# Performance work log

Measured on AMD Instinct MI355X. Metric: run time of the kernel, lower is better.

The kernel has to match this reference:

```python
import jax, jax.numpy as jnp
import numpy as np

B, T, L, D = 2, 16, 256, 1152
NH, HD = 16, 72
MLP_H = int(int(D * 4.0) * 2 / 3)  # 3072, per SwiGLUFFN


def _rms(x, w, eps=1e-6):
    return x * jax.lax.rsqrt(jnp.mean(jnp.square(x), axis=-1, keepdims=True) + eps) * w


def _attn(x, qkv_w, qkv_b, qn, kn, proj_w, proj_b, nh):
    Bn, N, C = x.shape
    hd = C // nh
    qkv = (x @ qkv_w + qkv_b).reshape(Bn, N, 3, nh, hd)
    qkv = jnp.transpose(qkv, (2, 0, 3, 1, 4))  # [3, Bn, nh, N, hd]
    q, k, v = qkv[0], qkv[1], qkv[2]
    q = _rms(q, qn)
    k = _rms(k, kn)
    scores = jnp.einsum('bhnd,bhmd->bhnm', q, k) / jnp.sqrt(jnp.float32(hd))
    a = jax.nn.softmax(scores, axis=-1)
    o = jnp.einsum('bhnm,bhmd->bhnd', a, v)
    o = jnp.transpose(o, (0, 2, 1, 3)).reshape(Bn, N, C)
    return o @ proj_w + proj_b


def setup_inputs() -> dict:
    key = jax.random.key(0)
    ks = jax.random.split(key, 12)
    w = lambda k, shape: jax.random.normal(k, shape, jnp.float32) * 0.02
    return {
        'x': jax.random.normal(ks[0], (B, T, L, D), jnp.float32),
        'c': jax.random.normal(ks[1], (B, D), jnp.float32),
        'norm1_w': jnp.ones((D,), jnp.float32),
        'norm2_w': jnp.ones((D,), jnp.float32),
        'norm3_w': jnp.ones((D,), jnp.float32),
        'qn_s': jnp.ones((HD,), jnp.float32),
        'kn_s': jnp.ones((HD,), jnp.float32),
        'qkv_s_w': w(ks[2], (D, 3 * D)),
        'qkv_s_b': jnp.zeros((3 * D,), jnp.float32),
        'proj_s_w': w(ks[3], (D, D)),
        'proj_s_b': jnp.zeros((D,), jnp.float32),
        'qn_t': jnp.ones((HD,), jnp.float32),
        'kn_t': jnp.ones((HD,), jnp.float32),
        'qkv_t_w': w(ks[4], (D, 3 * D)),
        'qkv_t_b': jnp.zeros((3 * D,), jnp.float32),
        'proj_t_w': w(ks[5], (D, D)),
        'proj_t_b': jnp.zeros((D,), jnp.float32),
        'w12_w': w(ks[6], (D, 2 * MLP_H)),
        'w12_b': jnp.zeros((2 * MLP_H,), jnp.float32),
        'w3_w': w(ks[7], (MLP_H, D)),
        'w3_b': jnp.zeros((D,), jnp.float32),
        'ada_w': w(ks[8], (D, 9 * D)),
        'ada_b': jnp.zeros((9 * D,), jnp.float32),
    }


def reference(x, c, norm1_w, norm2_w, norm3_w,
              qn_s, kn_s, qkv_s_w, qkv_s_b, proj_s_w, proj_s_b,
              qn_t, kn_t, qkv_t_w, qkv_t_b, proj_t_w, proj_t_b,
              w12_w, w12_b, w3_w, w3_b, ada_w, ada_b):
    Bb, Tt, Ll, Dd = x.shape
    # adaLN_modulation: SiLU then Linear, chunk into 9 [B, D] tensors
    ch = (jax.nn.silu(c) @ ada_w + ada_b).reshape(Bb, 9, Dd)
    sh_s, sc_s, g_s = ch[:, 0], ch[:, 1], ch[:, 2]
    sh_t, sc_t, g_t = ch[:, 3], ch[:, 4], ch[:, 5]
    sh_m, sc_m, g_m = ch[:, 6], ch[:, 7], ch[:, 8]

    # spatial attention over L, folded batch B*T
    x_s = x.reshape(Bb * Tt, Ll, Dd)
    shs = jnp.repeat(sh_s, Tt, axis=0)[:, None, :]   # [B*T,1,D]
    scs = jnp.repeat(sc_s, Tt, axis=0)[:, None, :]
    gs = jnp.repeat(g_s, Tt, axis=0)[:, None, :]
    xn = _rms(x_s, norm1_w) * (1 + scs) + shs
    x_s = x_s + gs * _attn(xn, qkv_s_w, qkv_s_b, qn_s, kn_s, proj_s_w, proj_s_b, NH)
    x = x_s.reshape(Bb, Tt, Ll, Dd)

    # temporal attention over T, folded batch B*L
    x_t = jnp.transpose(x, (0, 2, 1, 3)).reshape(Bb * Ll, Tt, Dd)
    sht = jnp.repeat(sh_t, Ll, axis=0)[:, None, :]
    sct = jnp.repeat(sc_t, Ll, axis=0)[:, None, :]
    gt = jnp.repeat(g_t, Ll, axis=0)[:, None, :]
    xn = _rms(x_t, norm2_w) * (1 + sct) + sht
    x_t = x_t + gt * _attn(xn, qkv_t_w, qkv_t_b, qn_t, kn_t, proj_t_w, proj_t_b, NH)
    x = jnp.transpose(x_t.reshape(Bb, Ll, Tt, Dd), (0, 2, 1, 3))

    # SwiGLU MLP with adaLN modulate + gate
    xn = _rms(x, norm3_w) * (1 + sc_m[:, None, None, :]) + sh_m[:, None, None, :]
    x12 = xn @ w12_w + w12_b
    x1, x2 = jnp.split(x12, 2, axis=-1)
    mlp_out = (jax.nn.silu(x1) * x2) @ w3_w + w3_b
    x = x + g_m[:, None, None, :] * mlp_out
    return x
```

## Files before the change

### kernel.cpp

```cpp
#include <hip/hip_runtime.h>
#include <stdint.h>

typedef __bf16 bf16x8 __attribute__((ext_vector_type(8)));
typedef float f32x4 __attribute__((ext_vector_type(4)));

__device__ __forceinline__ float b2f(uint32_t u) {
  union { uint32_t i; float f; } v; v.i = u << 16; return v.f;
}
__device__ __forceinline__ uint16_t f2b(float f) {
  union { float f; uint32_t i; } v; v.f = f;
  uint32_t r = (v.i + 0x7fffu + ((v.i >> 16) & 1u)) >> 16;
  return (uint16_t)r;
}
__device__ __forceinline__ void unpack8(uint4 u, float* f) {
  f[0] = b2f(u.x & 0xffffu); f[1] = b2f(u.x >> 16);
  f[2] = b2f(u.y & 0xffffu); f[3] = b2f(u.y >> 16);
  f[4] = b2f(u.z & 0xffffu); f[5] = b2f(u.z >> 16);
  f[6] = b2f(u.w & 0xffffu); f[7] = b2f(u.w >> 16);
}

__device__ __forceinline__ void gl2lds16(const void* g, void* l) {
  __builtin_amdgcn_global_load_lds(
      (const __attribute__((address_space(1))) void*)g,
      (__attribute__((address_space(3))) void*)l, 16, 0, 0);
}

__global__ __launch_bounds__(256) void gemm_k(
    const uint16_t* __restrict__ A, int lda,
    const uint16_t* __restrict__ Bt,
    const float* __restrict__ bias,
    uint16_t* __restrict__ outb,
    float* __restrict__ outf, const float* __restrict__ resid,
    const float* __restrict__ gate,
    int N, int K, int mode)
{
  __shared__ __align__(16) uint16_t As[2][128 * 32];
  __shared__ __align__(16) uint16_t Bs[2][128 * 32];
  const int tid = threadIdx.x;
  const int xcd = blockIdx.x & 7;
  const int slot = blockIdx.x >> 3;
  const int mt = xcd * 8 + (slot & 7);
  const int nt = slot >> 3;
  const int row0 = mt * 128, col0 = nt * 128;

  const int lane = tid & 63, wave = tid >> 6;
  const int l15 = lane & 15, quad = lane >> 4;
  const int wm = (wave & 1) * 64, wn = (wave >> 1) * 64;

  f32x4 acc[4][4];
  const f32x4 zero = {0.f, 0.f, 0.f, 0.f};
  for (int i = 0; i < 4; i++)
    for (int j = 0; j < 4; j++)
      acc[i][j] = zero;

  const int rseg = wave * 32 + (lane >> 2);
  const int kseg8 = (((lane & 3) ^ ((lane >> 2) & 3) ^ ((lane >> 4) & 3))) * 8;
  const uint16_t* gA = A + (size_t)(row0 + rseg) * lda + kseg8;
  const uint16_t* gB = Bt + (size_t)(col0 + rseg) * K + kseg8;
  const size_t rowA16 = (size_t)16 * lda;
  const size_t rowB16 = (size_t)16 * K;
  const int woff = wave * 2048;

  const int gsw = ((quad ^ (l15 & 3) ^ ((l15 >> 2) & 3))) * 8;

  gl2lds16(gA,          (char*)As[0] + woff);
  gl2lds16(gA + rowA16, (char*)As[0] + woff + 1024);
  gl2lds16(gB,          (char*)Bs[0] + woff);
  gl2lds16(gB + rowB16, (char*)Bs[0] + woff + 1024);

  for (int k0 = 0; k0 < K; k0 += 32) {
    const int cur = (k0 >> 5) & 1;
    __syncthreads();
    if (k0 + 32 < K) {
      const int nxt = cur ^ 1;
      gl2lds16(gA + k0 + 32,          (char*)As[nxt] + woff);
      gl2lds16(gA + rowA16 + k0 + 32, (char*)As[nxt] + woff + 1024);
      gl2lds16(gB + k0 + 32,          (char*)Bs[nxt] + woff);
      gl2lds16(gB + rowB16 + k0 + 32, (char*)Bs[nxt] + woff + 1024);
    }

    bf16x8 af[4], bfr[4];
#pragma unroll
    for (int i = 0; i < 4; i++) {
      af[i]  = *(const bf16x8*)&As[cur][(wm + i * 16 + l15) * 32 + gsw];
      bfr[i] = *(const bf16x8*)&Bs[cur][(wn + i * 16 + l15) * 32 + gsw];
    }
#pragma unroll
    for (int mi = 0; mi < 4; mi++)
#pragma unroll
      for (int ni = 0; ni < 4; ni++)
        acc[mi][ni] = __builtin_amdgcn_mfma_f32_16x16x32_bf16(af[mi], bfr[ni], acc[mi][ni], 0, 0, 0);
  }

#pragma unroll
  for (int mi = 0; mi < 4; mi++) {
#pragma unroll
    for (int ni = 0; ni < 4; ni++) {
      const int colg = col0 + wn + ni * 16 + l15;
      const float bv = bias ? bias[colg] : 0.f;
#pragma unroll
      for (int i = 0; i < 4; i++) {
        const int rowg = row0 + wm + mi * 16 + quad * 4 + i;
        const float v = acc[mi][ni][i] + bv;
        const size_t idx = (size_t)rowg * N + colg;
        if (mode == 0) {
          outb[idx] = f2b(v);
        } else {
          const int b = rowg >> 12;
          outf[idx] = resid[idx] + gate[b * 10368 + colg] * v;
        }
      }
    }
  }
}

__global__ __launch_bounds__(512, 2) void gemm256_sw_k(
    const uint16_t* __restrict__ A, int lda,
    const uint16_t* __restrict__ Bt,
    const float* __restrict__ bias,
    uint16_t* __restrict__ outh,
    int K)
{
  __shared__ __align__(16) uint16_t L[65536];
  const int tid = threadIdx.x;
  const int lane = tid & 63, wave = tid >> 6;
  const int l15 = lane & 15, quad = lane >> 4;
  const int wm = (wave >> 2) * 128, wn = (wave & 3) * 64;

  const int xcd = blockIdx.x & 7;
  const int slot = blockIdx.x >> 3;
  const int mt = xcd * 4 + (slot & 3);
  const int nt = slot >> 2;
  const int row0 = mt * 256, col0 = nt * 256;

  const int NTk = K >> 6;

  const uint16_t* Ag = A + (size_t)row0 * lda;
  const uint16_t* Bg = Bt + (size_t)col0 * K;

  const int sX = (lane & 7) ^ (lane >> 3);
  const int laneRowA = lane >> 3;
  const int laneK8A = sX * 8;
  const int laneRowB = 2 * (lane >> 3) + ((sX >> 2) & 1);
  const int laneK8B = (sX & 3) * 8;
  const int rA0 = ((wave * 16) & 63) + (((wave * 16) >> 6) << 7);
  const int rB0 = wave * 32;

#define STAGE_A(BUF, SUB, KT) do { \
    const uint16_t* g_ = Ag + (size_t)(rA0 + (SUB) * 64 + laneRowA) * lda + (size_t)(KT) * 64 + laneK8A; \
    uint16_t* l_ = (uint16_t*)&L[(BUF) * 32768 + (rA0 + (SUB) * 64) * 64]; \
    gl2lds16(g_, l_); \
    gl2lds16(g_ + (size_t)8 * lda, l_ + 512); \
  } while (0)

#define STAGE_B(BUF, HALF, KT) do { \
    const uint16_t* g_ = Bg + (size_t)(rB0 + laneRowB) * K + (size_t)(KT) * 64 + (HALF) * 32 + laneK8B; \
    uint16_t* l_ = (uint16_t*)&L[(BUF) * 32768 + 16384 + (HALF) * 8192 + rB0 * 32]; \
    gl2lds16(g_, l_); \
    gl2lds16(g_ + (size_t)16 * K, l_ + 512); \
  } while (0)

  f32x4 acc[8][4];
#pragma unroll
  for (int i = 0; i < 8; i++)
#pragma unroll
    for (int j = 0; j < 4; j++)
      acc[i][j] = (f32x4){0.f, 0.f, 0.f, 0.f};

  bf16x8 a_[4], b_[4];

#define PHASE(CUR, KK, QM, READB, STAGE_STMT, VM_STMT) do { \
    _Pragma("unroll") for (int mi = 0; mi < 4; mi++) \
      a_[mi] = *(const bf16x8*)&L[(CUR) * 32768 + (wm + (QM) * 64 + mi * 16 + l15) * 64 + \
                                  ((((KK) * 4 + quad) ^ (l15 & 7)) * 8)]; \
    if (READB) { \
      _Pragma("unroll") for (int ni = 0; ni < 4; ni++) \
        b_[ni] = *(const bf16x8*)&L[(CUR) * 32768 + 16384 + (KK) * 8192 + \
                                    ((wn >> 1) + ni * 8 + (l15 >> 1)) * 64 + \
                                    ((((((l15 & 1) << 2) | quad)) ^ (l15 >> 1)) * 8)]; \
    } \
    STAGE_STMT; \
    __builtin_amdgcn_sched_barrier(0); \
    __builtin_amdgcn_s_barrier(); \
    asm volatile("s_waitcnt lgkmcnt(0)" ::: "memory"); \
    __builtin_amdgcn_sched_barrier(0); \
    __builtin_amdgcn_s_setprio(1); \
    _Pragma("unroll") for (int mi = 0; mi < 4; mi++) \
      _Pragma("unroll") for (int ni = 0; ni < 4; ni++) \
        acc[(QM) * 4 + mi][ni] = __builtin_amdgcn_mfma_f32_16x16x32_bf16( \
            a_[mi], b_[ni], acc[(QM) * 4 + mi][ni], 0, 0, 0); \
    __builtin_amdgcn_s_setprio(0); \
    __builtin_amdgcn_sched_barrier(0); \
    VM_STMT; \
    __builtin_amdgcn_sched_barrier(0); \
    __builtin_amdgcn_s_barrier(); \
    __builtin_amdgcn_sched_barrier(0); \
  } while (0)

#define TILE(CUR, T) do { \
    PHASE(CUR, 0, 0, 1, { if ((T) + 1 < NTk) STAGE_B((CUR) ^ 1, 1, (T) + 1); }, {}); \
    PHASE(CUR, 0, 1, 0, { if ((T) + 1 < NTk) STAGE_A((CUR) ^ 1, 1, (T) + 1); }, {}); \
    PHASE(CUR, 1, 0, 1, { if ((T) + 2 < NTk) STAGE_B((CUR), 0, (T) + 2); }, {}); \
    PHASE(CUR, 1, 1, 0, { if ((T) + 2 < NTk) STAGE_A((CUR), 0, (T) + 2); }, \
      { if ((T) + 2 < NTk) { asm volatile("s_waitcnt vmcnt(4)" ::: "memory"); } \
        else               { asm volatile("s_waitcnt vmcnt(0)" ::: "memory"); } }); \
  } while (0)

  STAGE_A(0, 0, 0); STAGE_A(0, 1, 0); STAGE_B(0, 0, 0); STAGE_B(0, 1, 0);
  STAGE_A(1, 0, 1); STAGE_B(1, 0, 1);
  asm volatile("s_waitcnt vmcnt(4)" ::: "memory");
  __builtin_amdgcn_sched_barrier(0);
  __builtin_amdgcn_s_barrier();
  __builtin_amdgcn_sched_barrier(0);

  for (int t = 0; t < NTk; t += 2) {
    TILE(0, t);
    TILE(1, t + 1);
  }

#undef PHASE
#undef TILE
#undef STAGE_A
#undef STAGE_B

#pragma unroll
  for (int mi = 0; mi < 8; mi++) {
#pragma unroll
    for (int ni = 0; ni < 4; ni++) {
      const int colg = col0 + wn + ni * 16 + l15;
      const float bv = bias[(colg & 1) * 3072 + (colg >> 1)];
      const int hcol = ((col0 + wn + ni * 16) >> 1) + (l15 >> 1);
#pragma unroll
      for (int i = 0; i < 4; i++) {
        const int rowg = row0 + wm + mi * 16 + quad * 4 + i;
        const float v = acc[mi][ni][i] + bv;
        const float o = __shfl_xor(v, 1);
        if ((l15 & 1) == 0) {
          const float hres = v / (1.f + __expf(-v)) * o;
          outh[(size_t)rowg * 3072 + hcol] = f2b(hres);
        }
      }
    }
  }
}

__global__ __launch_bounds__(256) void rmsnorm_k(
    const float* __restrict__ x, const float* __restrict__ w,
    const float* __restrict__ chv, int shsel, int scsel,
    uint16_t* __restrict__ xn)
{
  const int row = blockIdx.x;
  const int b = row >> 12;
  const int tid = threadIdx.x;
  const float4* x4 = (const float4*)(x + (size_t)row * 1152);
  float4 a = x4[tid];
  float ss = a.x * a.x + a.y * a.y + a.z * a.z + a.w * a.w;
  float4 a2 = {0.f, 0.f, 0.f, 0.f};
  if (tid < 32) {
    a2 = x4[256 + tid];
    ss += a2.x * a2.x + a2.y * a2.y + a2.z * a2.z + a2.w * a2.w;
  }
  for (int off = 32; off > 0; off >>= 1) ss += __shfl_down(ss, off);
  __shared__ float red[4];
  if ((tid & 63) == 0) red[tid >> 6] = ss;
  __syncthreads();
  const float tot = red[0] + red[1] + red[2] + red[3];
  const float rs = rsqrtf(tot * (1.f / 1152.f) + 1e-6f);
  const float4* w4 = (const float4*)w;
  const float4* sh4 = (const float4*)(chv + b * 10368 + shsel * 1152);
  const float4* sc4 = (const float4*)(chv + b * 10368 + scsel * 1152);
  uint2* xo = (uint2*)(xn + (size_t)row * 1152);
  auto proc = [&](float4 av, int idx) {
    const float4 wv = w4[idx], shv = sh4[idx], scv = sc4[idx];
    const float r0 = av.x * rs * wv.x * (1.f + scv.x) + shv.x;
    const float r1 = av.y * rs * wv.y * (1.f + scv.y) + shv.y;
    const float r2 = av.z * rs * wv.z * (1.f + scv.z) + shv.z;
    const float r3 = av.w * rs * wv.w * (1.f + scv.w) + shv.w;
    uint2 o;
    o.x = (uint32_t)f2b(r0) | ((uint32_t)f2b(r1) << 16);
    o.y = (uint32_t)f2b(r2) | ((uint32_t)f2b(r3) << 16);
    xo[idx] = o;
  };
  proc(a, tid);
  if (tid < 32) proc(a2, 256 + tid);
}

__global__ __launch_bounds__(256) void qknorm_k(
    uint16_t* __restrict__ qkv, const float* __restrict__ qn, const float* __restrict__ kn)
{
  const int tid = threadIdx.x;
  const int rl = tid >> 5, unit = tid & 31;
  const int h = unit & 15, isK = unit >> 4;
  const size_t row = (size_t)blockIdx.x * 8 + rl;
  uint16_t* p = qkv + row * 3456 + isK * 1152 + h * 72;
  const float* w = isK ? kn : qn;
  float v[72];
#pragma unroll
  for (int i = 0; i < 9; i++) unpack8(((const uint4*)p)[i], v + i * 8);
  float ss = 0.f;
#pragma unroll
  for (int d = 0; d < 72; d++) ss += v[d] * v[d];
  const float rs = rsqrtf(ss * (1.f / 72.f) + 1e-6f);
#pragma unroll
  for (int d = 0; d < 72; d++) p[d] = f2b(v[d] * rs * w[d]);
}

#define AK_STRIDE 104
#define VT_STRIDE 88
#define PS_STRIDE 72
__global__ __launch_bounds__(256) void attn_s_k(
    const uint16_t* __restrict__ qkv, uint16_t* __restrict__ out)
{
  __shared__ __align__(16) uint16_t Ks[64 * AK_STRIDE];
  __shared__ __align__(16) uint16_t Vt[80 * VT_STRIDE];
  __shared__ __align__(16) uint16_t Ps[4 * 64 * PS_STRIDE];
  const int bh = blockIdx.x;
  const int bt = bh >> 4, h = bh & 15;
  const int tid = threadIdx.x;
  const int lane = tid & 63, wave = tid >> 6;
  const int l15 = lane & 15, quad = lane >> 4;
  const size_t rowbase = (size_t)bt * 256;
  const float scale = 0.1178511301977579f;

  union { uint4 u; bf16x8 v; } zu; zu.u = make_uint4(0, 0, 0, 0);
  const bf16x8 zero8 = zu.v;

  bf16x8 qf[4][3];
#pragma unroll
  for (int mi = 0; mi < 4; mi++) {
    const uint16_t* qp = qkv + (rowbase + wave * 64 + mi * 16 + l15) * 3456 + h * 72;
    qf[mi][0] = *(const bf16x8*)(qp + quad * 8);
    qf[mi][1] = *(const bf16x8*)(qp + 32 + quad * 8);
    qf[mi][2] = (quad == 0) ? *(const bf16x8*)(qp + 64) : zero8;
  }

  f32x4 oacc[4][5];
#pragma unroll
  for (int mi = 0; mi < 4; mi++)
#pragma unroll
    for (int dt = 0; dt < 5; dt++)
      oacc[mi][dt] = (f32x4){0.f, 0.f, 0.f, 0.f};
  float mrun[4][4], lrun[4][4];
#pragma unroll
  for (int mi = 0; mi < 4; mi++)
#pragma unroll
    for (int i = 0; i < 4; i++) { mrun[mi][i] = -1e30f; lrun[mi][i] = 0.f; }

  uint16_t* psw = &Ps[wave * 64 * PS_STRIDE];

  for (int c = 0; c < 4; c++) {
    __syncthreads();
    for (int idx = tid; idx < 576; idx += 256) {
      const int rr = idx / 9, cc = idx - rr * 9;
      const uint16_t* kg = qkv + (rowbase + c * 64 + rr) * 3456 + 1152 + h * 72 + cc * 8;
      *(uint4*)&Ks[rr * AK_STRIDE + cc * 8] = *(const uint4*)kg;
      uint4 vv = *(const uint4*)(kg + 1152);
      const uint16_t* e = (const uint16_t*)&vv;
#pragma unroll
      for (int j = 0; j < 8; j++) Vt[(cc * 8 + j) * VT_STRIDE + rr] = e[j];
    }
    __syncthreads();

    f32x4 s[4][4];
#pragma unroll
    for (int mi = 0; mi < 4; mi++)
#pragma unroll
      for (int ni = 0; ni < 4; ni++)
        s[mi][ni] = (f32x4){0.f, 0.f, 0.f, 0.f};
#pragma unroll
    for (int ni = 0; ni < 4; ni++) {
      bf16x8 kf0 = *(const bf16x8*)&Ks[(ni * 16 + l15) * AK_STRIDE + quad * 8];
      bf16x8 kf1 = *(const bf16x8*)&Ks[(ni * 16 + l15) * AK_STRIDE + 32 + quad * 8];
      bf16x8 kf2 = (quad == 0) ? *(const bf16x8*)&Ks[(ni * 16 + l15) * AK_STRIDE + 64] : zero8;
#pragma unroll
      for (int mi = 0; mi < 4; mi++) {
        s[mi][ni] = __builtin_amdgcn_mfma_f32_16x16x32_bf16(qf[mi][0], kf0, s[mi][ni], 0, 0, 0);
        s[mi][ni] = __builtin_amdgcn_mfma_f32_16x16x32_bf16(qf[mi][1], kf1, s[mi][ni], 0, 0, 0);
        s[mi][ni] = __builtin_amdgcn_mfma_f32_16x16x32_bf16(qf[mi][2], kf2, s[mi][ni], 0, 0, 0);
      }
    }

#pragma unroll
    for (int mi = 0; mi < 4; mi++) {
#pragma unroll
      for (int i = 0; i < 4; i++) {
        float mx = fmaxf(fmaxf(s[mi][0][i], s[mi][1][i]), fmaxf(s[mi][2][i], s[mi][3][i])) * scale;
#pragma unroll
        for (int d = 1; d < 16; d <<= 1) mx = fmaxf(mx, __shfl_xor(mx, d));
        const float mnew = fmaxf(mrun[mi][i], mx);
        const float corr = __expf(mrun[mi][i] - mnew);
        mrun[mi][i] = mnew;
        float psum = 0.f;
#pragma unroll
        for (int ni = 0; ni < 4; ni++) {
          const float p = __expf(s[mi][ni][i] * scale - mnew);
          s[mi][ni][i] = p;
          psum += p;
        }
#pragma unroll
        for (int d = 1; d < 16; d <<= 1) psum += __shfl_xor(psum, d);
        lrun[mi][i] = lrun[mi][i] * corr + psum;
#pragma unroll
        for (int dt = 0; dt < 5; dt++) oacc[mi][dt][i] *= corr;
      }
    }

#pragma unroll
    for (int mi = 0; mi < 4; mi++)
#pragma unroll
      for (int ni = 0; ni < 4; ni++)
#pragma unroll
        for (int i = 0; i < 4; i++)
          psw[(mi * 16 + quad * 4 + i) * PS_STRIDE + ni * 16 + l15] = f2b(s[mi][ni][i]);

#pragma unroll
    for (int kk = 0; kk < 2; kk++) {
      bf16x8 pf[4];
#pragma unroll
      for (int mi = 0; mi < 4; mi++)
        pf[mi] = *(const bf16x8*)&psw[(mi * 16 + l15) * PS_STRIDE + kk * 32 + quad * 8];
#pragma unroll
      for (int dt = 0; dt < 5; dt++) {
        bf16x8 vf = *(const bf16x8*)&Vt[(dt * 16 + l15) * VT_STRIDE + kk * 32 + quad * 8];
#pragma unroll
        for (int mi = 0; mi < 4; mi++)
          oacc[mi][dt] = __builtin_amdgcn_mfma_f32_16x16x32_bf16(pf[mi], vf, oacc[mi][dt], 0, 0, 0);
      }
    }
  }

#pragma unroll
  for (int mi = 0; mi < 4; mi++) {
#pragma unroll
    for (int i = 0; i < 4; i++) {
      const float inv = 1.f / lrun[mi][i];
      const size_t orow = rowbase + wave * 64 + mi * 16 + quad * 4 + i;
#pragma unroll
      for (int dt = 0; dt < 5; dt++) {
        const int d = dt * 16 + l15;
        if (d < 72) out[orow * 1152 + h * 72 + d] = f2b(oacc[mi][dt][i] * inv);
      }
    }
  }
}

__global__ __launch_bounds__(128) void attn_t_k(
    const uint16_t* __restrict__ qkv, uint16_t* __restrict__ out)
{
  const int blk = blockIdx.x;
  const int bl = blk >> 1, hg = blk & 1;
  const int b = bl >> 8, l = bl & 255;
  const int tid = threadIdx.x;
  const int hh = tid >> 4, tq = tid & 15;
  const int h = hg * 8 + hh;
  __shared__ __align__(16) uint16_t kb[8 * 16 * 72];
  __shared__ __align__(16) uint16_t vb[8 * 16 * 72];

#pragma unroll
  for (int it = 0; it < 9; it++) {
    const int idx = tid + it * 128;
    const int rowL = idx / 9, cc = idx % 9;
    const int hhL = rowL >> 4, tL = rowL & 15;
    const size_t grow = (size_t)b * 4096 + (size_t)tL * 256 + l;
    const int colk = 1152 + (hg * 8 + hhL) * 72 + cc * 8;
    ((uint4*)&kb[rowL * 72])[cc] = *(const uint4*)(qkv + grow * 3456 + colk);
    ((uint4*)&vb[rowL * 72])[cc] = *(const uint4*)(qkv + grow * 3456 + colk + 1152);
  }
  __syncthreads();

  float q[72];
  const size_t qrow = (size_t)b * 4096 + (size_t)tq * 256 + l;
  {
    const uint16_t* qp = qkv + qrow * 3456 + h * 72;
#pragma unroll
    for (int i = 0; i < 9; i++) unpack8(((const uint4*)qp)[i], q + i * 8);
  }
  const float scale = 0.1178511301977579f;
  float s[16];
#pragma unroll
  for (int m = 0; m < 16; m++) {
    const uint4* kr = (const uint4*)&kb[(hh * 16 + m) * 72];
    float a = 0.f;
#pragma unroll
    for (int i = 0; i < 9; i++) {
      float kf[8]; unpack8(kr[i], kf);
#pragma unroll
      for (int j = 0; j < 8; j++) a += q[i * 8 + j] * kf[j];
    }
    s[m] = a * scale;
  }
  float mx = -1e30f;
#pragma unroll
  for (int m = 0; m < 16; m++) mx = fmaxf(mx, s[m]);
  float sum = 0.f;
#pragma unroll
  for (int m = 0; m < 16; m++) { s[m] = __expf(s[m] - mx); sum += s[m]; }
  const float inv = 1.f / sum;
  float o[72];
#pragma unroll
  for (int d = 0; d < 72; d++) o[d] = 0.f;
#pragma unroll
  for (int m = 0; m < 16; m++) {
    const float p = s[m];
    const uint4* vr = (const uint4*)&vb[(hh * 16 + m) * 72];
#pragma unroll
    for (int i = 0; i < 9; i++) {
      float vf[8]; unpack8(vr[i], vf);
#pragma unroll
      for (int j = 0; j < 8; j++) o[i * 8 + j] += p * vf[j];
    }
  }
  uint16_t* op = out + qrow * 1152 + h * 72;
#pragma unroll
  for (int d = 0; d < 72; d++) op[d] = f2b(o[d] * inv);
}

__global__ __launch_bounds__(256) void transcvt_k(
    const float* __restrict__ in, uint16_t* __restrict__ out, int K, int N)
{
  __shared__ float t[32][33];
  const int n0 = blockIdx.x * 32, k0 = blockIdx.y * 32;
  const int tx = threadIdx.x & 31, ty = threadIdx.x >> 5;
#pragma unroll
  for (int i = 0; i < 32; i += 8)
    t[ty + i][tx] = in[(size_t)(k0 + ty + i) * N + n0 + tx];
  __syncthreads();
#pragma unroll
  for (int i = 0; i < 32; i += 8)
    out[(size_t)(n0 + ty + i) * K + k0 + tx] = f2b(t[tx][ty + i]);
}

__global__ __launch_bounds__(256) void transcvt_w12i_k(
    const float* __restrict__ in, uint16_t* __restrict__ out)
{
  __shared__ float t[32][33];
  const int n0 = blockIdx.x * 32, k0 = blockIdx.y * 32;
  const int tx = threadIdx.x & 31, ty = threadIdx.x >> 5;
  const int scol = ((tx & 1) * 3072) + (n0 >> 1) + (tx >> 1);
#pragma unroll
  for (int i = 0; i < 32; i += 8)
    t[ty + i][tx] = in[(size_t)(k0 + ty + i) * 6144 + scol];
  __syncthreads();
#pragma unroll
  for (int i = 0; i < 32; i += 8)
    out[(size_t)(n0 + ty + i) * 1152 + k0 + tx] = f2b(t[tx][ty + i]);
}

__global__ void siluc_k(const float* __restrict__ c, float* __restrict__ cs) {
  const int i = blockIdx.x * 256 + threadIdx.x;
  if (i < 2304) { const float v = c[i]; cs[i] = v / (1.f + __expf(-v)); }
}

#define ADA_KS 18
#define ADA_RK 64
__global__ __launch_bounds__(256) void ada_part_k(
    const float* __restrict__ cs, const float* __restrict__ W,
    float* __restrict__ part)
{
  const int col = blockIdx.x * 256 + threadIdx.x;
  const int ks = blockIdx.y;
  const int k0 = ks * ADA_RK;
  __shared__ float sc0[ADA_RK], sc1[ADA_RK];
  if (threadIdx.x < ADA_RK) sc0[threadIdx.x] = cs[k0 + threadIdx.x];
  else if (threadIdx.x < 2 * ADA_RK) sc1[threadIdx.x - ADA_RK] = cs[1152 + k0 + threadIdx.x - ADA_RK];
  __syncthreads();
  if (col >= 10368) return;
  const float* Wp = W + (size_t)k0 * 10368 + col;
  float s0 = 0.f, s1 = 0.f;
#pragma unroll 8
  for (int r = 0; r < ADA_RK; r++) {
    const float wv = Wp[(size_t)r * 10368];
    s0 += sc0[r] * wv;
    s1 += sc1[r] * wv;
  }
  part[(size_t)(ks * 2 + 0) * 10368 + col] = s0;
  part[(size_t)(ks * 2 + 1) * 10368 + col] = s1;
}

__global__ __launch_bounds__(256) void ada_reduce_k(
    const float* __restrict__ part, const float* __restrict__ bias,
    float* __restrict__ chv)
{
  const int col = blockIdx.x * 256 + threadIdx.x;
  if (col >= 10368) return;
  float s0 = bias[col], s1 = bias[col];
#pragma unroll
  for (int ks = 0; ks < ADA_KS; ks++) {
    s0 += part[(size_t)(ks * 2 + 0) * 10368 + col];
    s1 += part[(size_t)(ks * 2 + 1) * 10368 + col];
  }
  chv[col] = s0;
  chv[10368 + col] = s1;
}

extern "C" void kernel_launch(void* const* d_in, const int* in_sizes, int n_in,
                              void* d_out, int out_size, void* d_ws, size_t ws_size,
                              hipStream_t stream)
{
  const float* Xin     = (const float*)d_in[0];
  const float* c_in    = (const float*)d_in[1];
  const float* norm1w  = (const float*)d_in[2];
  const float* norm2w  = (const float*)d_in[3];
  const float* norm3w  = (const float*)d_in[4];
  const float* qn_s    = (const float*)d_in[5];
  const float* kn_s    = (const float*)d_in[6];
  const float* qkv_s_w = (const float*)d_in[7];
  const float* qkv_s_b = (const float*)d_in[8];
  const float* proj_s_w= (const float*)d_in[9];
  const float* proj_s_b= (const float*)d_in[10];
  const float* qn_t    = (const float*)d_in[11];
  const float* kn_t    = (const float*)d_in[12];
  const float* qkv_t_w = (const float*)d_in[13];
  const float* qkv_t_b = (const float*)d_in[14];
  const float* proj_t_w= (const float*)d_in[15];
  const float* proj_t_b= (const float*)d_in[16];
  const float* w12_w   = (const float*)d_in[17];
  const float* w12_b   = (const float*)d_in[18];
  const float* w3_w    = (const float*)d_in[19];
  const float* w3_b    = (const float*)d_in[20];
  const float* ada_w   = (const float*)d_in[21];
  const float* ada_b   = (const float*)d_in[22];

  float* X = (float*)d_out;

  char* wsb = (char*)d_ws; size_t off = 0;
  auto alloc = [&](size_t bytes) -> void* {
    void* p = wsb + off; off += bytes; off = (off + 255) & ~(size_t)255; return p;
  };
  uint16_t* XN    = (uint16_t*)alloc((size_t)8192 * 1152 * 2);
  uint16_t* QKV   = (uint16_t*)alloc((size_t)8192 * 3456 * 2);
  uint16_t* H     = QKV;
  uint16_t* WqkvS = (uint16_t*)alloc((size_t)3456 * 1152 * 2);
  uint16_t* WprojS= (uint16_t*)alloc((size_t)1152 * 1152 * 2);
  uint16_t* WqkvT = (uint16_t*)alloc((size_t)3456 * 1152 * 2);
  uint16_t* WprojT= (uint16_t*)alloc((size_t)1152 * 1152 * 2);
  uint16_t* W12T  = (uint16_t*)alloc((size_t)6144 * 1152 * 2);
  uint16_t* W3T   = (uint16_t*)alloc((size_t)1152 * 3072 * 2);
  float* CH = (float*)alloc((size_t)2 * 10368 * 4);
  float* CS = (float*)alloc((size_t)2 * 1152 * 4);
  float* APART = (float*)alloc((size_t)ADA_KS * 2 * 10368 * 4);

  siluc_k<<<9, 256, 0, stream>>>(c_in, CS);
  ada_part_k<<<dim3(41, ADA_KS), 256, 0, stream>>>(CS, ada_w, APART);
  ada_reduce_k<<<41, 256, 0, stream>>>(APART, ada_b, CH);

  transcvt_k<<<dim3(3456 / 32, 1152 / 32), 256, 0, stream>>>(qkv_s_w, WqkvS, 1152, 3456);
  transcvt_k<<<dim3(1152 / 32, 1152 / 32), 256, 0, stream>>>(proj_s_w, WprojS, 1152, 1152);
  transcvt_k<<<dim3(3456 / 32, 1152 / 32), 256, 0, stream>>>(qkv_t_w, WqkvT, 1152, 3456);
  transcvt_k<<<dim3(1152 / 32, 1152 / 32), 256, 0, stream>>>(proj_t_w, WprojT, 1152, 1152);
  transcvt_w12i_k<<<dim3(6144 / 32, 1152 / 32), 256, 0, stream>>>(w12_w, W12T);
  transcvt_k<<<dim3(1152 / 32, 3072 / 32), 256, 0, stream>>>(w3_w, W3T, 3072, 1152);

  rmsnorm_k<<<8192, 256, 0, stream>>>(Xin, norm1w, CH, 0, 1, XN);
  gemm_k<<<27 * 64, 256, 0, stream>>>(XN, 1152, WqkvS, qkv_s_b, QKV, nullptr, nullptr, nullptr,
                                      3456, 1152, 0);
  qknorm_k<<<1024, 256, 0, stream>>>(QKV, qn_s, kn_s);
  attn_s_k<<<512, 256, 0, stream>>>(QKV, XN);
  gemm_k<<<9 * 64, 256, 0, stream>>>(XN, 1152, WprojS, proj_s_b, nullptr, X, Xin, CH + 2 * 1152,
                                     1152, 1152, 1);

  rmsnorm_k<<<8192, 256, 0, stream>>>(X, norm2w, CH, 3, 4, XN);
  gemm_k<<<27 * 64, 256, 0, stream>>>(XN, 1152, WqkvT, qkv_t_b, QKV, nullptr, nullptr, nullptr,
                                      3456, 1152, 0);
  qknorm_k<<<1024, 256, 0, stream>>>(QKV, qn_t, kn_t);
  attn_t_k<<<1024, 128, 0, stream>>>(QKV, XN);
  gemm_k<<<9 * 64, 256, 0, stream>>>(XN, 1152, WprojT, proj_t_b, nullptr, X, X, CH + 5 * 1152,
                                     1152, 1152, 1);

  rmsnorm_k<<<8192, 256, 0, stream>>>(X, norm3w, CH, 6, 7, XN);
  gemm256_sw_k<<<32 * 24, 512, 0, stream>>>(XN, 1152, W12T, w12_b, H, 1152);
  gemm_k<<<9 * 64, 256, 0, stream>>>(H, 3072, W3T, w3_b, nullptr, X, X, CH + 8 * 1152,
                                     1152, 3072, 1);
}
```

Baseline: 976.1 us.

## Fuse q/k RMSNorm into attention kernels and regroup SwiGLU weight interleave

```diff
diff --git a/kernel.cpp b/kernel.cpp
--- a/kernel.cpp
+++ b/kernel.cpp
@@ -17,6 +17,14 @@
   f[2] = b2f(u.y & 0xffffu); f[3] = b2f(u.y >> 16);
   f[4] = b2f(u.z & 0xffffu); f[5] = b2f(u.z >> 16);
   f[6] = b2f(u.w & 0xffffu); f[7] = b2f(u.w >> 16);
+}
+__device__ __forceinline__ bf16x8 pack8(const float* f) {
+  union { uint4 u; bf16x8 v; } r;
+  r.u.x = (uint32_t)f2b(f[0]) | ((uint32_t)f2b(f[1]) << 16);
+  r.u.y = (uint32_t)f2b(f[2]) | ((uint32_t)f2b(f[3]) << 16);
+  r.u.z = (uint32_t)f2b(f[4]) | ((uint32_t)f2b(f[5]) << 16);
+  r.u.w = (uint32_t)f2b(f[6]) | ((uint32_t)f2b(f[7]) << 16);
+  return r.v;
 }
 
 __device__ __forceinline__ void gl2lds16(const void* g, void* l) {
@@ -223,22 +231,21 @@
 #undef STAGE_A
 #undef STAGE_B
 
+  const int hbase = ((col0 + wn) >> 6) * 32;
 #pragma unroll
   for (int mi = 0; mi < 8; mi++) {
 #pragma unroll
-    for (int ni = 0; ni < 4; ni++) {
-      const int colg = col0 + wn + ni * 16 + l15;
-      const float bv = bias[(colg & 1) * 3072 + (colg >> 1)];
-      const int hcol = ((col0 + wn + ni * 16) >> 1) + (l15 >> 1);
+    for (int ni = 0; ni < 2; ni++) {
+      const int p = hbase + ni * 16 + l15;
+      const float b1 = bias[p];
+      const float b2 = bias[3072 + p];
 #pragma unroll
       for (int i = 0; i < 4; i++) {
         const int rowg = row0 + wm + mi * 16 + quad * 4 + i;
-        const float v = acc[mi][ni][i] + bv;
-        const float o = __shfl_xor(v, 1);
-        if ((l15 & 1) == 0) {
-          const float hres = v / (1.f + __expf(-v)) * o;
-          outh[(size_t)rowg * 3072 + hcol] = f2b(hres);
-        }
+        const float v1 = acc[mi][ni][i] + b1;
+        const float v2 = acc[mi][ni + 2][i] + b2;
+        const float hres = v1 / (1.f + __expf(-v1)) * v2;
+        outh[(size_t)rowg * 3072 + p] = f2b(hres);
       }
     }
   }
@@ -285,31 +292,12 @@
   if (tid < 32) proc(a2, 256 + tid);
 }
 
-__global__ __launch_bounds__(256) void qknorm_k(
-    uint16_t* __restrict__ qkv, const float* __restrict__ qn, const float* __restrict__ kn)
-{
-  const int tid = threadIdx.x;
-  const int rl = tid >> 5, unit = tid & 31;
-  const int h = unit & 15, isK = unit >> 4;
-  const size_t row = (size_t)blockIdx.x * 8 + rl;
-  uint16_t* p = qkv + row * 3456 + isK * 1152 + h * 72;
-  const float* w = isK ? kn : qn;
-  float v[72];
-#pragma unroll
-  for (int i = 0; i < 9; i++) unpack8(((const uint4*)p)[i], v + i * 8);
-  float ss = 0.f;
-#pragma unroll
-  for (int d = 0; d < 72; d++) ss += v[d] * v[d];
-  const float rs = rsqrtf(ss * (1.f / 72.f) + 1e-6f);
-#pragma unroll
-  for (int d = 0; d < 72; d++) p[d] = f2b(v[d] * rs * w[d]);
-}
-
 #define AK_STRIDE 104
 #define VT_STRIDE 88
 #define PS_STRIDE 72
 __global__ __launch_bounds__(256) void attn_s_k(
-    const uint16_t* __restrict__ qkv, uint16_t* __restrict__ out)
+    const uint16_t* __restrict__ qkv, uint16_t* __restrict__ out,
+    const float* __restrict__ qn, const float* __restrict__ kn)
 {
   __shared__ __align__(16) uint16_t Ks[64 * AK_STRIDE];
   __shared__ __align__(16) uint16_t Vt[80 * VT_STRIDE];
@@ -325,13 +313,42 @@
   union { uint4 u; bf16x8 v; } zu; zu.u = make_uint4(0, 0, 0, 0);
   const bf16x8 zero8 = zu.v;
 
+  float qw0[8], qw1[8], qw2[8];
+#pragma unroll
+  for (int j = 0; j < 8; j++) {
+    qw0[j] = qn[quad * 8 + j];
+    qw1[j] = qn[32 + quad * 8 + j];
+    qw2[j] = (quad == 0) ? qn[64 + j] : 0.f;
+  }
+  const int knpart = tid & 3;
+  float knw[18];
+#pragma unroll
+  for (int j = 0; j < 18; j++) knw[j] = kn[knpart * 18 + j];
+
   bf16x8 qf[4][3];
 #pragma unroll
   for (int mi = 0; mi < 4; mi++) {
     const uint16_t* qp = qkv + (rowbase + wave * 64 + mi * 16 + l15) * 3456 + h * 72;
-    qf[mi][0] = *(const bf16x8*)(qp + quad * 8);
-    qf[mi][1] = *(const bf16x8*)(qp + 32 + quad * 8);
-    qf[mi][2] = (quad == 0) ? *(const bf16x8*)(qp + 64) : zero8;
+    float f0[8], f1[8], f2[8];
+    unpack8(((const uint4*)qp)[quad], f0);
+    unpack8(((const uint4*)qp)[4 + quad], f1);
+    uint4 u2 = (quad == 0) ? ((const uint4*)qp)[8] : make_uint4(0, 0, 0, 0);
+    unpack8(u2, f2);
+    float ss = 0.f;
+#pragma unroll
+    for (int j = 0; j < 8; j++) ss += f0[j] * f0[j] + f1[j] * f1[j] + f2[j] * f2[j];
+    ss += __shfl_xor(ss, 16);
+    ss += __shfl_xor(ss, 32);
+    const float rs = rsqrtf(ss * (1.f / 72.f) + 1e-6f);
+#pragma unroll
+    for (int j = 0; j < 8; j++) {
+      f0[j] *= rs * qw0[j];
+      f1[j] *= rs * qw1[j];
+      f2[j] *= rs * qw2[j];
+    }
+    qf[mi][0] = pack8(f0);
+    qf[mi][1] = pack8(f1);
+    qf[mi][2] = (quad == 0) ? pack8(f2) : zero8;
   }
 
   f32x4 oacc[4][5];
@@ -361,6 +378,21 @@
     }
     __syncthreads();
 
+    {
+      const int r = tid >> 2;
+      uint16_t* kr = &Ks[r * AK_STRIDE + knpart * 18];
+      float loc[18];
+      float ss = 0.f;
+#pragma unroll
+      for (int j = 0; j < 18; j++) { loc[j] = b2f(kr[j]); ss += loc[j] * loc[j]; }
+      ss += __shfl_xor(ss, 1);
+      ss += __shfl_xor(ss, 2);
+      const float rs = rsqrtf(ss * (1.f / 72.f) + 1e-6f);
+#pragma unroll
+      for (int j = 0; j < 18; j++) kr[j] = f2b(loc[j] * rs * knw[j]);
+    }
+    __syncthreads();
+
     f32x4 s[4][4];
 #pragma unroll
     for (int mi = 0; mi < 4; mi++)
@@ -445,7 +477,8 @@
 }
 
 __global__ __launch_bounds__(128) void attn_t_k(
-    const uint16_t* __restrict__ qkv, uint16_t* __restrict__ out)
+    const uint16_t* __restrict__ qkv, uint16_t* __restrict__ out,
+    const float* __restrict__ qn, const float* __restrict__ kn)
 {
   const int blk = blockIdx.x;
   const int bl = blk >> 1, hg = blk & 1;
@@ -468,12 +501,40 @@
   }
   __syncthreads();
 
+  {
+    uint16_t* kr = &kb[tid * 72];
+    float ss = 0.f;
+#pragma unroll
+    for (int i = 0; i < 9; i++) {
+      float f[8]; unpack8(((const uint4*)kr)[i], f);
+#pragma unroll
+      for (int j = 0; j < 8; j++) ss += f[j] * f[j];
+    }
+    const float rs = rsqrtf(ss * (1.f / 72.f) + 1e-6f);
+#pragma unroll
+    for (int i = 0; i < 9; i++) {
+      float f[8]; unpack8(((const uint4*)kr)[i], f);
+#pragma unroll
+      for (int j = 0; j < 8; j++) f[j] *= rs * kn[i * 8 + j];
+      union { uint4 u; bf16x8 v; } r;
+      r.v = pack8(f);
+      ((uint4*)kr)[i] = r.u;
+    }
+  }
+  __syncthreads();
+
   float q[72];
   const size_t qrow = (size_t)b * 4096 + (size_t)tq * 256 + l;
   {
     const uint16_t* qp = qkv + qrow * 3456 + h * 72;
 #pragma unroll
     for (int i = 0; i < 9; i++) unpack8(((const uint4*)qp)[i], q + i * 8);
+    float ssq = 0.f;
+#pragma unroll
+    for (int d = 0; d < 72; d++) ssq += q[d] * q[d];
+    const float rsq = rsqrtf(ssq * (1.f / 72.f) + 1e-6f);
+#pragma unroll
+    for (int d = 0; d < 72; d++) q[d] *= rsq * qn[d];
   }
   const float scale = 0.1178511301977579f;
   float s[16];
@@ -536,7 +597,7 @@
   __shared__ float t[32][33];
   const int n0 = blockIdx.x * 32, k0 = blockIdx.y * 32;
   const int tx = threadIdx.x & 31, ty = threadIdx.x >> 5;
-  const int scol = ((tx & 1) * 3072) + (n0 >> 1) + (tx >> 1);
+  const int scol = ((n0 & 32) ? 3072 : 0) + ((n0 >> 6) << 5) + tx;
 #pragma unroll
   for (int i = 0; i < 32; i += 8)
     t[ty + i][tx] = in[(size_t)(k0 + ty + i) * 6144 + scol];
@@ -654,16 +715,14 @@
   rmsnorm_k<<<8192, 256, 0, stream>>>(Xin, norm1w, CH, 0, 1, XN);
   gemm_k<<<27 * 64, 256, 0, stream>>>(XN, 1152, WqkvS, qkv_s_b, QKV, nullptr, nullptr, nullptr,
                                       3456, 1152, 0);
-  qknorm_k<<<1024, 256, 0, stream>>>(QKV, qn_s, kn_s);
-  attn_s_k<<<512, 256, 0, stream>>>(QKV, XN);
+  attn_s_k<<<512, 256, 0, stream>>>(QKV, XN, qn_s, kn_s);
   gemm_k<<<9 * 64, 256, 0, stream>>>(XN, 1152, WprojS, proj_s_b, nullptr, X, Xin, CH + 2 * 1152,
                                      1152, 1152, 1);
 
   rmsnorm_k<<<8192, 256, 0, stream>>>(X, norm2w, CH, 3, 4, XN);
   gemm_k<<<27 * 64, 256, 0, stream>>>(XN, 1152, WqkvT, qkv_t_b, QKV, nullptr, nullptr, nullptr,
                                       3456, 1152, 0);
-  qknorm_k<<<1024, 256, 0, stream>>>(QKV, qn_t, kn_t);
-  attn_t_k<<<1024, 128, 0, stream>>>(QKV, XN);
+  attn_t_k<<<1024, 128, 0, stream>>>(QKV, XN, qn_t, kn_t);
   gemm_k<<<9 * 64, 256, 0, stream>>>(XN, 1152, WprojT, proj_t_b, nullptr, X, X, CH + 5 * 1152,
                                      1152, 1152, 1);
 
```

New measurement: 915.8 us. 6.2% less time.
